# Kernel optimization log

Measured on AMD Instinct MI355X. Metric: run time of the kernel, lower is better.

Reference implementation:

```python
import jax, jax.numpy as jnp
import numpy as np

THRESHOLD = 0.5
NEG_POS_RATIO = 3


def cxcycz_to_xyz(c):
    return jnp.concatenate([c[..., :3] - c[..., 3:] / 2, c[..., :3] + c[..., 3:] / 2], axis=-1)


def xyz_to_cxcycz(x):
    return jnp.concatenate([(x[..., :3] + x[..., 3:]) / 2, x[..., 3:] - x[..., :3]], axis=-1)


def cxcycz_to_gcxgcygcz(c, priors):
    # SSD offset encoding (variance 0.1 / 0.2), 3D version
    return jnp.concatenate([
        (c[..., :3] - priors[..., :3]) / (priors[..., 3:] / 10.0),
        jnp.log(c[..., 3:] / priors[..., 3:]) * 5.0,
    ], axis=-1)


def jaccard3d(a, b):
    # a: [n,6] xyz boxes, b: [m,6] xyz boxes -> [n,m] IoU
    lo = jnp.maximum(a[:, None, :3], b[None, :, :3])
    hi = jnp.minimum(a[:, None, 3:], b[None, :, 3:])
    inter = jnp.prod(jnp.clip(hi - lo, 0.0, None), axis=-1)
    va = jnp.prod(a[:, 3:] - a[:, :3], axis=-1)
    vb = jnp.prod(b[:, 3:] - b[:, :3], axis=-1)
    return inter / (va[:, None] + vb[None, :] - inter)


def setup_inputs() -> dict:
    key = jax.random.key(0)
    ks = jax.random.split(key, 6)
    B, P, n_obj, n_classes = 16, 131072, 16, 2
    predicted_locs = jax.random.normal(ks[0], (B, P, 6), jnp.float32)
    predicted_scores = jax.random.normal(ks[1], (B, P, n_classes), jnp.float32)
    ctr = jax.random.uniform(ks[2], (B, n_obj, 3), minval=0.2, maxval=0.8)
    sz = jax.random.uniform(ks[3], (B, n_obj, 3), minval=0.05, maxval=0.2)
    boxes = jnp.concatenate([ctr - sz / 2, ctr + sz / 2], axis=-1)
    labels = jnp.ones((B, n_obj), jnp.int32)  # single foreground class (lesion)
    pctr = jax.random.uniform(ks[4], (P, 3), minval=0.0, maxval=1.0)
    psz = jax.random.uniform(ks[5], (P, 3), minval=0.05, maxval=0.3)
    priors_cxcycz = jnp.concatenate([pctr, psz], axis=-1)
    return {
        'predicted_locs': predicted_locs,
        'predicted_scores': predicted_scores,
        'boxes': boxes,
        'labels': labels,
        'priors_cxcycz': priors_cxcycz,
    }


def reference(predicted_locs, predicted_scores, boxes, labels, priors_cxcycz):
    B, P, n_classes = predicted_scores.shape
    n_obj = boxes.shape[1]
    priors_xyz = cxcycz_to_xyz(priors_cxcycz)

    def match(boxes_i, labels_i):
        ov = jaccard3d(boxes_i, priors_xyz)              # [n_obj, P]
        overlap_fp = ov.max(axis=0)                      # best overlap per prior
        object_fp = jnp.argmax(ov, axis=0)               # best object per prior
        prior_fo = jnp.argmax(ov, axis=1)                # best prior per object
        # force each object's best prior to be matched to that object
        object_fp = object_fp.at[prior_fo].set(jnp.arange(n_obj))
        overlap_fp = overlap_fp.at[prior_fo].set(1.0)
        lab = jnp.where(overlap_fp < THRESHOLD, 0, labels_i[object_fp])
        tl = cxcycz_to_gcxgcygcz(xyz_to_cxcycz(boxes_i[object_fp]), priors_cxcycz)
        return lab, tl

    true_classes, true_locs = jax.vmap(match)(boxes, labels)  # [B,P], [B,P,6]

    pos = true_classes > 0                               # [B,P]
    n_pos = pos.sum(axis=1)                              # [B]
    total_pos = n_pos.sum()

    # L1Loss(mean) over positive rows of [*,6]
    loc_abs = jnp.abs(predicted_locs - true_locs).sum(axis=-1)   # [B,P]
    loc_loss = (loc_abs * pos).sum() / (total_pos * 6).astype(predicted_locs.dtype)

    # per-prior cross-entropy
    logp = jax.nn.log_softmax(predicted_scores, axis=-1)
    conf_all = -jnp.take_along_axis(logp, true_classes[..., None], axis=-1)[..., 0]
    conf_all = jnp.where(true_classes < 0, 0.0, conf_all)  # ignored priors (soft mode only)
    conf_pos_sum = (conf_all * pos).sum()

    # hard-negative mining: zero out positives, sort each row descending, take top 3*n_pos
    conf_neg = jnp.where(pos, 0.0, conf_all)
    conf_neg_sorted = -jnp.sort(-conf_neg, axis=1)
    hard = jnp.arange(P)[None, :] < (NEG_POS_RATIO * n_pos)[:, None]
    conf_loss = (jnp.where(hard, conf_neg_sorted, 0.0).sum() + conf_pos_sum) / total_pos.astype(predicted_scores.dtype)
    return conf_loss, loc_loss
```

## Files before the change

kernel.cpp:

```cpp
#include <hip/hip_runtime.h>
#include <math.h>

#define LB 32


__device__ __forceinline__ unsigned long long umax64(unsigned long long a,
                                                     unsigned long long b) {
  return a > b ? a : b;
}

template <int NOBJ, bool FULL>
__global__ __launch_bounds__(256, 8) void mbl_match(
    const float* __restrict__ boxes, const float* __restrict__ priors,
    unsigned long long* __restrict__ prior_fo, unsigned char* __restrict__ best_u8,
    int P, int n_obj) {
  const int b = blockIdx.y;
  const int tid = threadIdx.x;
  __shared__ float4 s_box[NOBJ][2];
  __shared__ unsigned s_tr[16][264];
  for (int i = tid; i < NOBJ; i += 256) {
    float4 v0, v1;
    if (i < n_obj) {
      const float* bx = boxes + ((size_t)b * n_obj + i) * 6;
      const float l0 = bx[0], l1 = bx[1], l2 = bx[2];
      const float h0 = bx[3], h1 = bx[4], h2 = bx[5];
      v0 = make_float4(l0, l1, l2, h0);
      v1 = make_float4(h1, h2, ((h0 - l0) * (h1 - l1)) * (h2 - l2), 0.f);
    } else {
      v0 = make_float4(3e18f, 3e18f, 3e18f, 1e18f);
      v1 = make_float4(1e18f, 1e18f, 0.f, 0.f);
    }
    s_box[i][0] = v0;
    s_box[i][1] = v1;
  }
  __syncthreads();

  const int pbase = blockIdx.x * 256;
  const int p = pbase + tid;
  float lo0, lo1, lo2, hi0, hi1, hi2, vb;
  if (FULL || p < P) {
    const float2 q0 = *(const float2*)(priors + (size_t)p * 6);
    const float2 q1 = *(const float2*)(priors + (size_t)p * 6 + 2);
    const float2 q2 = *(const float2*)(priors + (size_t)p * 6 + 4);
    lo0 = q0.x - q1.y * 0.5f; hi0 = q0.x + q1.y * 0.5f;
    lo1 = q0.y - q2.x * 0.5f; hi1 = q0.y + q2.x * 0.5f;
    lo2 = q1.x - q2.y * 0.5f; hi2 = q1.x + q2.y * 0.5f;
    vb = (q1.y * q2.x) * q2.y;
  } else {
    lo0 = lo1 = lo2 = 3e18f;
    hi0 = hi1 = hi2 = 3e18f;
    vb = 0.f;
  }

  const unsigned msk = ~(unsigned)(NOBJ - 1);
  unsigned pk = 0u;

  for (int o0 = 0; o0 < NOBJ; o0 += 16) {
    if (o0) __syncthreads();
#pragma unroll
    for (int oo = 0; oo < 16; ++oo) {
      const int o = o0 + oo;
      const float4 c0 = s_box[o][0];
      const float4 c1 = s_box[o][1];
      const float d0 = fminf(c0.w, hi0) - fmaxf(c0.x, lo0);
      const float d1 = fminf(c1.x, hi1) - fmaxf(c0.y, lo1);
      const float d2 = fminf(c1.y, hi2) - fmaxf(c0.z, lo2);
      const float inter = (fmaxf(d0, 0.f) * fmaxf(d1, 0.f)) * fmaxf(d2, 0.f);
      const float un = (c1.z + vb) - inter;
      const float iou = inter * __builtin_amdgcn_rcpf(un);
      s_tr[oo][tid] = __float_as_uint(iou);
      const unsigned cand =
          (__float_as_uint(iou) & msk) | (unsigned)(NOBJ - 1 - o);
      pk = max(pk, cand);
    }
    __syncthreads();
    const int obj = tid >> 4, j = tid & 15;
    unsigned long long m = 0ULL;
#pragma unroll
    for (int i = 0; i < 16; ++i) {
      const int col = j + 16 * i;
      const unsigned long long x =
          ((unsigned long long)s_tr[obj][col] << 32) |
          (0xFFFFFFFFu - (unsigned)(pbase + col));
      m = umax64(m, x);
    }
#pragma unroll
    for (int off = 1; off < 16; off <<= 1)
      m = umax64(m, __shfl_xor(m, off, 64));
    if (j == 0) {
      const int o = o0 + obj;
      if (o < n_obj) atomicMax(&prior_fo[(size_t)b * 64 + o], m);
    }
  }

  if (FULL || p < P) {
    const int bo = (NOBJ - 1) - (int)(pk & (unsigned)(NOBJ - 1));
    best_u8[(size_t)b * P + p] =
        (unsigned char)((unsigned)bo | (pk >= 0x3F000000u ? 0x80u : 0u));
  }
}

template <int CC>
__global__ __launch_bounds__(256) void mbl_loss(
    const float* __restrict__ locs, const float* __restrict__ scores,
    const float* __restrict__ boxes, const int* __restrict__ labels,
    const float* __restrict__ priors, const unsigned long long* __restrict__ prior_fo,
    const unsigned char* __restrict__ best_u8, float* __restrict__ conf_neg,
    unsigned* __restrict__ hist0, int* __restrict__ n_pos,
    double* __restrict__ pconf, double* __restrict__ ploc, int P, int n_obj,
    int C) {
  const int b = blockIdx.y;
  const int tid = threadIdx.x;
  __shared__ float s_box[64][6];
  __shared__ int s_lab[64];
  __shared__ unsigned s_fo[64];
  __shared__ unsigned s_hist[4096];
  for (int i = tid; i < 4096; i += 256) s_hist[i] = 0u;
  for (int i = tid; i < n_obj * 6; i += 256)
    s_box[i / 6][i % 6] = boxes[(size_t)b * n_obj * 6 + i];
  for (int i = tid; i < n_obj; i += 256) {
    s_lab[i] = labels[(size_t)b * n_obj + i];
    s_fo[i] = 0xFFFFFFFFu - (unsigned)(prior_fo[(size_t)b * 64 + i] & 0xFFFFFFFFull);
  }
  __syncthreads();

  unsigned fo_r[16];
  const bool small_obj = (n_obj <= 16);
  if (small_obj) {
#pragma unroll
    for (int o = 0; o < 16; ++o) fo_r[o] = (o < n_obj) ? s_fo[o] : 0xFFFFFFFEu;
  }

  int np_l = 0;
  double cf_l = 0.0, lc_l = 0.0;

  if (CC == 2 && (P & 1) == 0) {
    const int P2 = P >> 1;
    const int chunk = (P2 + (int)gridDim.x - 1) / (int)gridDim.x;
    const int start = blockIdx.x * chunk;
    const int end = min(start + chunk, P2);
    for (int q = start + tid; q < end; q += 256) {
      const float4 sc = *(const float4*)(scores + ((size_t)b * P2 + q) * 4);
      const unsigned short bpp =
          *(const unsigned short*)(best_u8 + (size_t)b * P + 2 * q);
      float cn2[2];
#pragma unroll
      for (int e = 0; e < 2; ++e) {
        const int p = 2 * q + e;
        const unsigned bp = e ? (bpp >> 8) : (bpp & 0xFFu);
        int obj = bp & 0x7F;
        int posf = (int)(bp >> 7);
        if (small_obj) {
#pragma unroll
          for (int o = 0; o < 16; ++o)
            if (fo_r[o] == (unsigned)p) { obj = o; posf = 1; }
        } else {
          for (int o = 0; o < n_obj; ++o)
            if (s_fo[o] == (unsigned)p) { obj = o; posf = 1; }
        }
        const int lab = posf ? s_lab[obj] : 0;
        const float sx = e ? sc.z : sc.x;
        const float sy = e ? sc.w : sc.y;
        const float mm = fmaxf(sx, sy);
        const float conf =
            (lab < 0) ? 0.f
                      : (mm + __logf(__expf(sx - mm) + __expf(sy - mm)) -
                         ((lab == 0) ? sx : sy));
        float cn = conf;
        if (lab > 0) {
          np_l++;
          cf_l += (double)conf;
          const float* pr = priors + (size_t)p * 6;
          const float* pl = locs + ((size_t)b * P + p) * 6;
          float ls = 0.f;
          for (int i = 0; i < 3; ++i) {
            const float c0 = (s_box[obj][i] + s_box[obj][i + 3]) * 0.5f;
            const float szb = s_box[obj][i + 3] - s_box[obj][i];
            const float g = (c0 - pr[i]) / (pr[i + 3] / 10.0f);
            const float g2 = logf(szb / pr[i + 3]) * 5.0f;
            ls += fabsf(pl[i] - g) + fabsf(pl[i + 3] - g2);
          }
          lc_l += (double)ls;
          cn = 0.f;
        }
        cn2[e] = cn;
        atomicAdd(&s_hist[__float_as_uint(cn) >> 20], 1u);
      }
      *(float2*)(conf_neg + (size_t)b * P + 2 * q) = make_float2(cn2[0], cn2[1]);
    }
  } else {
    const int chunk = (P + (int)gridDim.x - 1) / (int)gridDim.x;
    const int start = blockIdx.x * chunk;
    const int end = min(start + chunk, P);
    for (int p = start + tid; p < end; p += 256) {
      const unsigned char bp = best_u8[(size_t)b * P + p];
      int obj = bp & 0x7F;
      int posf = bp >> 7;
      for (int o = 0; o < n_obj; ++o)
        if (s_fo[o] == (unsigned)p) { obj = o; posf = 1; }
      const int lab = posf ? s_lab[obj] : 0;
      const float* sp = scores + ((size_t)b * P + p) * C;
      float m = sp[0];
      for (int c = 1; c < C; ++c) m = fmaxf(m, sp[c]);
      float se = 0.f;
      for (int c = 0; c < C; ++c) se += __expf(sp[c] - m);
      const float conf = (lab < 0) ? 0.f : (m + __logf(se) - sp[lab]);
      float cn = conf;
      if (lab > 0) {
        np_l++;
        cf_l += (double)conf;
        const float* pr = priors + (size_t)p * 6;
        const float* pl = locs + ((size_t)b * P + p) * 6;
        float ls = 0.f;
        for (int i = 0; i < 3; ++i) {
          const float c0 = (s_box[obj][i] + s_box[obj][i + 3]) * 0.5f;
          const float szb = s_box[obj][i + 3] - s_box[obj][i];
          const float g = (c0 - pr[i]) / (pr[i + 3] / 10.0f);
          const float g2 = logf(szb / pr[i + 3]) * 5.0f;
          ls += fabsf(pl[i] - g) + fabsf(pl[i + 3] - g2);
        }
        lc_l += (double)ls;
        cn = 0.f;
      }
      conf_neg[(size_t)b * P + p] = cn;
      atomicAdd(&s_hist[__float_as_uint(cn) >> 20], 1u);
    }
  }

  __shared__ int r_np[256];
  __shared__ double r_c[256];
  __shared__ double r_l[256];
  r_np[tid] = np_l;
  r_c[tid] = cf_l;
  r_l[tid] = lc_l;
  __syncthreads();
  for (int s = 128; s > 0; s >>= 1) {
    if (tid < s) {
      r_np[tid] += r_np[tid + s];
      r_c[tid] += r_c[tid + s];
      r_l[tid] += r_l[tid + s];
    }
    __syncthreads();
  }
  if (tid == 0 && r_np[0] > 0) {
    atomicAdd(&n_pos[b], r_np[0]);
    atomicAdd(&pconf[b], r_c[0]);
    atomicAdd(&ploc[b], r_l[0]);
  }
  for (int i = tid; i < 4096; i += 256)
    if (s_hist[i]) atomicAdd(&hist0[(size_t)b * 4096 + i], s_hist[i]);
}

template <int BINS>
__device__ void block_select(const unsigned* __restrict__ h, int remk,
                             unsigned* s_scan, int* s_out, unsigned* sel,
                             int* remk_o) {
  constexpr int BPT = BINS / 256;
  const int t = threadIdx.x;
  if (t == 0) { s_out[0] = BINS - 1; s_out[1] = 0; }
  unsigned mb[BPT];
  unsigned s = 0;
#pragma unroll
  for (int i = 0; i < BPT; ++i) { mb[i] = h[t * BPT + i]; s += mb[i]; }
  unsigned incl = s;
  s_scan[t] = incl;
  __syncthreads();
  for (int off = 1; off < 256; off <<= 1) {
    const unsigned add = (t >= off) ? s_scan[t - off] : 0u;
    __syncthreads();
    incl += add;
    s_scan[t] = incl;
    __syncthreads();
  }
  const unsigned total = s_scan[255];
  const unsigned R = total - incl;
  if (remk > 0 && R < (unsigned)remk && R + s >= (unsigned)remk) {
    unsigned acc = R;
    int sel_i = t * BPT, rk = 0;
    bool done = false;
#pragma unroll
    for (int i = BPT - 1; i >= 0; --i) {
      if (!done && acc + mb[i] >= (unsigned)remk) {
        sel_i = t * BPT + i;
// ... 117 lines not shown
  const float* locs = (const float*)d_in[0];
  const float* scores = (const float*)d_in[1];
  const float* boxes = (const float*)d_in[2];
  const int* labels = (const int*)d_in[3];
  const float* priors = (const float*)d_in[4];

  const long long sz_locs = (long long)in_sizes[0];
  const long long sz_scores = (long long)in_sizes[1];
  const long long sz_priors = (long long)in_sizes[4];
  const int P = (int)(sz_priors / 6);
  const int B = (int)(sz_locs / sz_priors);
  const int n_obj = in_sizes[3] / B;
  const int C = (int)(sz_scores * 6 / sz_locs);

  char* ws = (char*)d_ws;
  size_t off = 0;
  double* pconf = (double*)(ws + off); off += (size_t)B * 8;
  double* ploc = (double*)(ws + off); off += (size_t)B * 8;
  double* phard = (double*)(ws + off); off += (size_t)B * 8;
  int* n_pos = (int*)(ws + off); off += ((size_t)B * 4 + 15) & ~(size_t)15;
  unsigned* counter = (unsigned*)(ws + off); off += 16;
  unsigned long long* prior_fo = (unsigned long long*)(ws + off);
  off += (size_t)B * 64 * 8;
  unsigned* hist0 = (unsigned*)(ws + off); off += (size_t)B * 4096 * 4;
  unsigned* hist1 = (unsigned*)(ws + off); off += (size_t)B * 4096 * 4;
  const size_t zero_bytes = off;
  float* conf_neg = (float*)(ws + off); off += ((size_t)B * P * 4 + 15) & ~(size_t)15;
  unsigned char* best_u8 = (unsigned char*)(ws + off);
  off += ((size_t)B * P + 15) & ~(size_t)15;
  (void)ws_size;

  hipMemsetAsync(d_ws, 0, zero_bytes, stream);

  const int nblk = (P + 255) / 256;
  const dim3 mgrid(nblk, B);
  const bool full = (P % 256) == 0;
  if (n_obj <= 16) {
    if (full) mbl_match<16, true><<<mgrid, 256, 0, stream>>>(boxes, priors, prior_fo, best_u8, P, n_obj);
    else      mbl_match<16, false><<<mgrid, 256, 0, stream>>>(boxes, priors, prior_fo, best_u8, P, n_obj);
  } else if (n_obj <= 32) {
    if (full) mbl_match<32, true><<<mgrid, 256, 0, stream>>>(boxes, priors, prior_fo, best_u8, P, n_obj);
    else      mbl_match<32, false><<<mgrid, 256, 0, stream>>>(boxes, priors, prior_fo, best_u8, P, n_obj);
  } else {
    if (full) mbl_match<64, true><<<mgrid, 256, 0, stream>>>(boxes, priors, prior_fo, best_u8, P, n_obj);
    else      mbl_match<64, false><<<mgrid, 256, 0, stream>>>(boxes, priors, prior_fo, best_u8, P, n_obj);
  }

  const dim3 lgrid(LB, B);
  if (C == 2)
    mbl_loss<2><<<lgrid, 256, 0, stream>>>(locs, scores, boxes, labels, priors,
                                           prior_fo, best_u8, conf_neg, hist0, n_pos,
                                           pconf, ploc, P, n_obj, C);
  else
    mbl_loss<0><<<lgrid, 256, 0, stream>>>(locs, scores, boxes, labels, priors,
                                           prior_fo, best_u8, conf_neg, hist0, n_pos,
                                           pconf, ploc, P, n_obj, C);

  mbl_hist1<<<lgrid, 256, 0, stream>>>(conf_neg, n_pos, hist0, hist1, P);
  mbl_sum<<<lgrid, 256, 0, stream>>>(conf_neg, n_pos, hist0, hist1, pconf, ploc,
                                     phard, counter, P, B, (float*)d_out);
}
```

Measured before the change: 102.9 us.

## Process two priors per thread in match kernel with scalar box loads

The match kernel now handles two priors per thread (a 512-prior tile) and loads the ground-truth boxes through readfirstlane scalar reads instead of a shared-memory box table. Objects are processed in passes of 8. Each thread first reduces its two priors' IoUs and records which one won in a bitmask, so the shared-memory transpose and the per-object block reduction are half the size. The aim is fewer blocks, less shared-memory traffic and fewer atomics per prior, at the cost of more registers, with the 8-occupancy launch bound dropped. The old mbl_match is left behind as a stub that no longer writes best_u8, and the launch sites call mbl_match2 instead.

```diff
diff --git a/kernel.cpp b/kernel.cpp
--- a/kernel.cpp
+++ b/kernel.cpp
@@ -1,6 +1,8 @@
 #include <hip/hip_runtime.h>
 #include <math.h>
 
+#define MITEMS 2
+#define TILE 512
 #define LB 32
 
 
@@ -8,95 +10,234 @@
                                                      unsigned long long b) {
   return a > b ? a : b;
 }
+__device__ __forceinline__ float rfl(float x) {
+  return __uint_as_float(__builtin_amdgcn_readfirstlane(__float_as_uint(x)));
+}
 
 template <int NOBJ, bool FULL>
-__global__ __launch_bounds__(256, 8) void mbl_match(
+__global__ __launch_bounds__(256) void mbl_match(
     const float* __restrict__ boxes, const float* __restrict__ priors,
     unsigned long long* __restrict__ prior_fo, unsigned char* __restrict__ best_u8,
     int P, int n_obj) {
   const int b = blockIdx.y;
   const int tid = threadIdx.x;
-  __shared__ float4 s_box[NOBJ][2];
-  __shared__ unsigned s_tr[16][264];
-  for (int i = tid; i < NOBJ; i += 256) {
-    float4 v0, v1;
-    if (i < n_obj) {
-      const float* bx = boxes + ((size_t)b * n_obj + i) * 6;
-      const float l0 = bx[0], l1 = bx[1], l2 = bx[2];
-      const float h0 = bx[3], h1 = bx[4], h2 = bx[5];
-      v0 = make_float4(l0, l1, l2, h0);
-      v1 = make_float4(h1, h2, ((h0 - l0) * (h1 - l1)) * (h2 - l2), 0.f);
+  __shared__ unsigned s_iou[8][264];
+  __shared__ unsigned s_kfl[264];
+
+  const int pbase = blockIdx.x * TILE;
+  float lo0[MITEMS], lo1[MITEMS], lo2[MITEMS], hi0[MITEMS], hi1[MITEMS],
+      hi2[MITEMS], vb[MITEMS];
+#pragma unroll
+  for (int k = 0; k < MITEMS; ++k) {
+    const int p = pbase + k * 256 + tid;
+    if (FULL || p < P) {
+      const float2 q0 = *(const float2*)(priors + (size_t)p * 6);
+      const float2 q1 = *(const float2*)(priors + (size_t)p * 6 + 2);
+      const float2 q2 = *(const float2*)(priors + (size_t)p * 6 + 4);
+      lo0[k] = q0.x - q1.y * 0.5f; hi0[k] = q0.x + q1.y * 0.5f;
+      lo1[k] = q0.y - q2.x * 0.5f; hi1[k] = q0.y + q2.x * 0.5f;
+      lo2[k] = q1.x - q2.y * 0.5f; hi2[k] = q1.x + q2.y * 0.5f;
+      vb[k] = (q1.y * q2.x) * q2.y;
     } else {
-      v0 = make_float4(3e18f, 3e18f, 3e18f, 1e18f);
-      v1 = make_float4(1e18f, 1e18f, 0.f, 0.f);
-    }
-    s_box[i][0] = v0;
-    s_box[i][1] = v1;
-  }
-  __syncthreads();
-
-  const int pbase = blockIdx.x * 256;
-  const int p = pbase + tid;
-  float lo0, lo1, lo2, hi0, hi1, hi2, vb;
-  if (FULL || p < P) {
-    const float2 q0 = *(const float2*)(priors + (size_t)p * 6);
-    const float2 q1 = *(const float2*)(priors + (size_t)p * 6 + 2);
-    const float2 q2 = *(const float2*)(priors + (size_t)p * 6 + 4);
-    lo0 = q0.x - q1.y * 0.5f; hi0 = q0.x + q1.y * 0.5f;
-    lo1 = q0.y - q2.x * 0.5f; hi1 = q0.y + q2.x * 0.5f;
-    lo2 = q1.x - q2.y * 0.5f; hi2 = q1.x + q2.y * 0.5f;
-    vb = (q1.y * q2.x) * q2.y;
-  } else {
-    lo0 = lo1 = lo2 = 3e18f;
-    hi0 = hi1 = hi2 = 3e18f;
-    vb = 0.f;
+      lo0[k] = lo1[k] = lo2[k] = 3e18f;
+      hi0[k] = hi1[k] = hi2[k] = 3e18f;
+      vb[k] = 0.f;
+    }
   }
 
   const unsigned msk = ~(unsigned)(NOBJ - 1);
   unsigned pk = 0u;
-
-  for (int o0 = 0; o0 < NOBJ; o0 += 16) {
-    if (o0) __syncthreads();
-#pragma unroll
-    for (int oo = 0; oo < 16; ++oo) {
-      const int o = o0 + oo;
-      const float4 c0 = s_box[o][0];
-      const float4 c1 = s_box[o][1];
-      const float d0 = fminf(c0.w, hi0) - fmaxf(c0.x, lo0);
-      const float d1 = fminf(c1.x, hi1) - fmaxf(c0.y, lo1);
-      const float d2 = fminf(c1.y, hi2) - fmaxf(c0.z, lo2);
-      const float inter = (fmaxf(d0, 0.f) * fmaxf(d1, 0.f)) * fmaxf(d2, 0.f);
-      const float un = (c1.z + vb) - inter;
-      const float iou = inter * __builtin_amdgcn_rcpf(un);
-      s_tr[oo][tid] = __float_as_uint(iou);
-      const unsigned cand =
-          (__float_as_uint(iou) & msk) | (unsigned)(NOBJ - 1 - o);
-      pk = max(pk, cand);
-    }
+  const float* bx = boxes + (size_t)b * n_obj * 6;
+
+  for (int pass = 0; pass < NOBJ / 8; ++pass) {
+    if (pass) __syncthreads();
+    float sl0[8], sl1[8], sl2[8], sh0[8], sh1[8], sh2[8], sv[8];
+#pragma unroll
+    for (int oo = 0; oo < 8; ++oo) {
+      const int o = pass * 8 + oo;
+      if (o < n_obj) {
+        const float* q = bx + (size_t)o * 6;
+        sl0[oo] = rfl(q[0]); sl1[oo] = rfl(q[1]); sl2[oo] = rfl(q[2]);
+        sh0[oo] = rfl(q[3]); sh1[oo] = rfl(q[4]); sh2[oo] = rfl(q[5]);
+        sv[oo] = rfl(((sh0[oo] - sl0[oo]) * (sh1[oo] - sl1[oo])) *
+                     (sh2[oo] - sl2[oo]));
+      } else {
+        sl0[oo] = sl1[oo] = sl2[oo] = 3e18f;
+        sh0[oo] = sh1[oo] = sh2[oo] = 3e18f;
+        sv[oo] = 0.f;
+      }
+    }
+
+    float piou[8];
+#pragma unroll
+    for (int oo = 0; oo < 8; ++oo) piou[oo] = 0.f;
+    unsigned kfl = 0u;
+
+#pragma unroll
+    for (int oo = 0; oo < 8; ++oo) {
+      const int o = pass * 8 + oo;
+#pragma unroll
+      for (int k = 0; k < MITEMS; ++k) {
+        const float d0 = fminf(sh0[oo], hi0[k]) - fmaxf(sl0[oo], lo0[k]);
+        const float d1 = fminf(sh1[oo], hi1[k]) - fmaxf(sl1[oo], lo1[k]);
+        const float d2 = fminf(sh2[oo], hi2[k]) - fmaxf(sl2[oo], lo2[k]);
+        const float inter = (fmaxf(d0, 0.f) * fmaxf(d1, 0.f)) * fmaxf(d2, 0.f);
+        const float un = (sv[oo] + vb[k]) - inter;
+        const float iou = inter * __builtin_amdgcn_rcpf(un);
+        const unsigned cand =
+            (__float_as_uint(iou) & msk) | (unsigned)(NOBJ - 1 - o);
+        pk = max(pk, cand);
+        const bool win = iou > piou[oo];
+        piou[oo] = win ? iou : piou[oo];
+        if (k > 0) kfl = win ? (kfl | (1u << oo)) : kfl;
+      }
+    }
+
+    s_kfl[tid] = kfl;
+#pragma unroll
+    for (int oo = 0; oo < 8; ++oo) s_iou[oo][tid] = __float_as_uint(piou[oo]);
     __syncthreads();
-    const int obj = tid >> 4, j = tid & 15;
+    const int obj8 = tid >> 5, j = tid & 31;
     unsigned long long m = 0ULL;
 #pragma unroll
-    for (int i = 0; i < 16; ++i) {
-      const int col = j + 16 * i;
-      const unsigned long long x =
-          ((unsigned long long)s_tr[obj][col] << 32) |
-          (0xFFFFFFFFu - (unsigned)(pbase + col));
-      m = umax64(m, x);
-    }
-#pragma unroll
-    for (int off = 1; off < 16; off <<= 1)
+    for (int i = 0; i < 8; ++i) {
+      const int col = j + 32 * i;
+      const unsigned ib = s_iou[obj8][col];
+      const unsigned kf = (s_kfl[col] >> obj8) & 1u;
+      const int p = pbase + (int)kf * 256 + col;
+      m = umax64(m, ((unsigned long long)ib << 32) |
+                        (0xFFFFFFFFu - (unsigned)p));
+    }
+#pragma unroll
+    for (int off = 1; off < 32; off <<= 1)
       m = umax64(m, __shfl_xor(m, off, 64));
     if (j == 0) {
-      const int o = o0 + obj;
+      const int o = pass * 8 + obj8;
       if (o < n_obj) atomicMax(&prior_fo[(size_t)b * 64 + o], m);
     }
   }
 
-  if (FULL || p < P) {
-    const int bo = (NOBJ - 1) - (int)(pk & (unsigned)(NOBJ - 1));
-    best_u8[(size_t)b * P + p] =
-        (unsigned char)((unsigned)bo | (pk >= 0x3F000000u ? 0x80u : 0u));
+#pragma unroll
+  for (int k = 0; k < MITEMS; ++k) {
+    const int p = pbase + k * 256 + tid;
+    if (FULL || p < P) {
+    }
+  }
+  (void)best_u8;
+}
+
+template <int NOBJ, bool FULL>
+__global__ __launch_bounds__(256) void mbl_match2(
+    const float* __restrict__ boxes, const float* __restrict__ priors,
+    unsigned long long* __restrict__ prior_fo, unsigned char* __restrict__ best_u8,
+    int P, int n_obj) {
+  const int b = blockIdx.y;
+  const int tid = threadIdx.x;
+  __shared__ unsigned s_iou[8][264];
+  __shared__ unsigned s_kfl[264];
+
+  const int pbase = blockIdx.x * TILE;
+  float lo0[MITEMS], lo1[MITEMS], lo2[MITEMS], hi0[MITEMS], hi1[MITEMS],
+      hi2[MITEMS], vb[MITEMS];
+#pragma unroll
+  for (int k = 0; k < MITEMS; ++k) {
+    const int p = pbase + k * 256 + tid;
+    if (FULL || p < P) {
+      const float2 q0 = *(const float2*)(priors + (size_t)p * 6);
+      const float2 q1 = *(const float2*)(priors + (size_t)p * 6 + 2);
+      const float2 q2 = *(const float2*)(priors + (size_t)p * 6 + 4);
+      lo0[k] = q0.x - q1.y * 0.5f; hi0[k] = q0.x + q1.y * 0.5f;
+      lo1[k] = q0.y - q2.x * 0.5f; hi1[k] = q0.y + q2.x * 0.5f;
+      lo2[k] = q1.x - q2.y * 0.5f; hi2[k] = q1.x + q2.y * 0.5f;
+      vb[k] = (q1.y * q2.x) * q2.y;
+    } else {
+      lo0[k] = lo1[k] = lo2[k] = 3e18f;
+      hi0[k] = hi1[k] = hi2[k] = 3e18f;
+      vb[k] = 0.f;
+    }
+  }
+
+  const unsigned msk = ~(unsigned)(NOBJ - 1);
+  unsigned pk[MITEMS];
+#pragma unroll
+  for (int k = 0; k < MITEMS; ++k) pk[k] = 0u;
+  const float* bx = boxes + (size_t)b * n_obj * 6;
+
+  for (int pass = 0; pass < NOBJ / 8; ++pass) {
+    if (pass) __syncthreads();
+    float sl0[8], sl1[8], sl2[8], sh0[8], sh1[8], sh2[8], sv[8];
+#pragma unroll
+    for (int oo = 0; oo < 8; ++oo) {
+      const int o = pass * 8 + oo;
+      if (o < n_obj) {
+        const float* q = bx + (size_t)o * 6;
+        sl0[oo] = rfl(q[0]); sl1[oo] = rfl(q[1]); sl2[oo] = rfl(q[2]);
+        sh0[oo] = rfl(q[3]); sh1[oo] = rfl(q[4]); sh2[oo] = rfl(q[5]);
+        sv[oo] = rfl(((sh0[oo] - sl0[oo]) * (sh1[oo] - sl1[oo])) *
+                     (sh2[oo] - sl2[oo]));
+      } else {
+        sl0[oo] = sl1[oo] = sl2[oo] = 3e18f;
+        sh0[oo] = sh1[oo] = sh2[oo] = 3e18f;
+        sv[oo] = 0.f;
+      }
+    }
+
+    float piou[8];
+#pragma unroll
+    for (int oo = 0; oo < 8; ++oo) piou[oo] = 0.f;
+    unsigned kfl = 0u;
+
+#pragma unroll
+    for (int oo = 0; oo < 8; ++oo) {
+      const int o = pass * 8 + oo;
+      const unsigned inv_o = (unsigned)(NOBJ - 1 - o);
+#pragma unroll
+      for (int k = 0; k < MITEMS; ++k) {
+        const float d0 = fminf(sh0[oo], hi0[k]) - fmaxf(sl0[oo], lo0[k]);
+        const float d1 = fminf(sh1[oo], hi1[k]) - fmaxf(sl1[oo], lo1[k]);
+        const float d2 = fminf(sh2[oo], hi2[k]) - fmaxf(sl2[oo], lo2[k]);
+        const float inter = (fmaxf(d0, 0.f) * fmaxf(d1, 0.f)) * fmaxf(d2, 0.f);
+        const float un = (sv[oo] + vb[k]) - inter;
+        const float iou = inter * __builtin_amdgcn_rcpf(un);
+        pk[k] = max(pk[k], (__float_as_uint(iou) & msk) | inv_o);
+        const bool win = iou > piou[oo];
+        piou[oo] = win ? iou : piou[oo];
+        if (k > 0) kfl = win ? (kfl | (1u << oo)) : kfl;
+      }
+    }
+
+    s_kfl[tid] = kfl;
+#pragma unroll
+    for (int oo = 0; oo < 8; ++oo) s_iou[oo][tid] = __float_as_uint(piou[oo]);
+    __syncthreads();
+    const int obj8 = tid >> 5, j = tid & 31;
+    unsigned long long m = 0ULL;
+#pragma unroll
+    for (int i = 0; i < 8; ++i) {
+      const int col = j + 32 * i;
+      const unsigned ib = s_iou[obj8][col];
+      const unsigned kf = (s_kfl[col] >> obj8) & 1u;
+      const int p = pbase + (int)kf * 256 + col;
+      m = umax64(m, ((unsigned long long)ib << 32) |
+                        (0xFFFFFFFFu - (unsigned)p));
+    }
+#pragma unroll
+    for (int off = 1; off < 32; off <<= 1)
+      m = umax64(m, __shfl_xor(m, off, 64));
+    if (j == 0) {
+      const int o = pass * 8 + obj8;
+      if (o < n_obj) atomicMax(&prior_fo[(size_t)b * 64 + o], m);
+    }
+  }
+
+#pragma unroll
+  for (int k = 0; k < MITEMS; ++k) {
+    const int p = pbase + k * 256 + tid;
+    if (FULL || p < P) {
+      const int bo = (NOBJ - 1) - (int)(pk[k] & (unsigned)(NOBJ - 1));
+      best_u8[(size_t)b * P + p] =
+          (unsigned char)((unsigned)bo | (pk[k] >= 0x3F000000u ? 0x80u : 0u));
+    }
   }
 }
 
@@ -432,18 +573,18 @@
 
   hipMemsetAsync(d_ws, 0, zero_bytes, stream);
 
-  const int nblk = (P + 255) / 256;
+  const int nblk = (P + TILE - 1) / TILE;
   const dim3 mgrid(nblk, B);
-  const bool full = (P % 256) == 0;
+  const bool full = (P % TILE) == 0;
   if (n_obj <= 16) {
-    if (full) mbl_match<16, true><<<mgrid, 256, 0, stream>>>(boxes, priors, prior_fo, best_u8, P, n_obj);
-    else      mbl_match<16, false><<<mgrid, 256, 0, stream>>>(boxes, priors, prior_fo, best_u8, P, n_obj);
+    if (full) mbl_match2<16, true><<<mgrid, 256, 0, stream>>>(boxes, priors, prior_fo, best_u8, P, n_obj);
+    else      mbl_match2<16, false><<<mgrid, 256, 0, stream>>>(boxes, priors, prior_fo, best_u8, P, n_obj);
   } else if (n_obj <= 32) {
-    if (full) mbl_match<32, true><<<mgrid, 256, 0, stream>>>(boxes, priors, prior_fo, best_u8, P, n_obj);
-    else      mbl_match<32, false><<<mgrid, 256, 0, stream>>>(boxes, priors, prior_fo, best_u8, P, n_obj);
+    if (full) mbl_match2<32, true><<<mgrid, 256, 0, stream>>>(boxes, priors, prior_fo, best_u8, P, n_obj);
+    else      mbl_match2<32, false><<<mgrid, 256, 0, stream>>>(boxes, priors, prior_fo, best_u8, P, n_obj);
   } else {
-    if (full) mbl_match<64, true><<<mgrid, 256, 0, stream>>>(boxes, priors, prior_fo, best_u8, P, n_obj);
-    else      mbl_match<64, false><<<mgrid, 256, 0, stream>>>(boxes, priors, prior_fo, best_u8, P, n_obj);
+    if (full) mbl_match2<64, true><<<mgrid, 256, 0, stream>>>(boxes, priors, prior_fo, best_u8, P, n_obj);
+    else      mbl_match2<64, false><<<mgrid, 256, 0, stream>>>(boxes, priors, prior_fo, best_u8, P, n_obj);
   }
 
   const dim3 lgrid(LB, B);
```

Result: faster. 97.96 us (-4.8%).

## Fuse prior matching with loss kernel and patch forced matches in a fixup pass

Applied to the files above, without the earlier changes.

The separate match and loss kernels are merged into one kernel. It computes IoU per prior against boxes held in scalar registers, then applies cross-entropy, localisation loss and the histogram update in the same pass. The per-object best prior is gathered with a per-thread running max and a single block reduction per group of eight objects, instead of a shared-memory transpose at every tile. Because the forced prior-to-object assignment is only known after all blocks finish, a small single-thread fixup kernel per batch then adjusts conf_neg, hist0, n_pos and the partial sums for those priors. This removes one kernel launch and the best_u8/conf_neg round trip, but the fixup runs serially and the grid is smaller (64×B blocks), which may reduce parallelism.

```diff
diff --git a/kernel.cpp b/kernel.cpp
--- a/kernel.cpp
+++ b/kernel.cpp
@@ -1,6 +1,7 @@
 #include <hip/hip_runtime.h>
 #include <math.h>
 
+#define LBF 64
 #define LB 32
 
 
@@ -8,174 +9,126 @@
                                                      unsigned long long b) {
   return a > b ? a : b;
 }
-
-template <int NOBJ, bool FULL>
-__global__ __launch_bounds__(256, 8) void mbl_match(
-    const float* __restrict__ boxes, const float* __restrict__ priors,
-    unsigned long long* __restrict__ prior_fo, unsigned char* __restrict__ best_u8,
-    int P, int n_obj) {
+__device__ __forceinline__ float rfl(float x) {
+  return __uint_as_float(__builtin_amdgcn_readfirstlane(__float_as_uint(x)));
+}
+
+template <int CC>
+__global__ __launch_bounds__(256) void mbl_fused(
+    const float* __restrict__ locs, const float* __restrict__ scores,
+    const float* __restrict__ boxes, const int* __restrict__ labels,
+    const float* __restrict__ priors, unsigned long long* __restrict__ prior_fo,
+    unsigned char* __restrict__ best_u8, float* __restrict__ conf_neg,
+    unsigned* __restrict__ hist0, int* __restrict__ n_pos,
+    double* __restrict__ pconf, double* __restrict__ ploc, int P, int n_obj,
+    int chunks, int C) {
   const int b = blockIdx.y;
   const int tid = threadIdx.x;
-  __shared__ float4 s_box[NOBJ][2];
-  __shared__ unsigned s_tr[16][264];
-  for (int i = tid; i < NOBJ; i += 256) {
-    float4 v0, v1;
-    if (i < n_obj) {
-      const float* bx = boxes + ((size_t)b * n_obj + i) * 6;
-      const float l0 = bx[0], l1 = bx[1], l2 = bx[2];
-      const float h0 = bx[3], h1 = bx[4], h2 = bx[5];
-      v0 = make_float4(l0, l1, l2, h0);
-      v1 = make_float4(h1, h2, ((h0 - l0) * (h1 - l1)) * (h2 - l2), 0.f);
-    } else {
-      v0 = make_float4(3e18f, 3e18f, 3e18f, 1e18f);
-      v1 = make_float4(1e18f, 1e18f, 0.f, 0.f);
-    }
-    s_box[i][0] = v0;
-    s_box[i][1] = v1;
-  }
-  __syncthreads();
-
-  const int pbase = blockIdx.x * 256;
-  const int p = pbase + tid;
-  float lo0, lo1, lo2, hi0, hi1, hi2, vb;
-  if (FULL || p < P) {
-    const float2 q0 = *(const float2*)(priors + (size_t)p * 6);
-    const float2 q1 = *(const float2*)(priors + (size_t)p * 6 + 2);
-    const float2 q2 = *(const float2*)(priors + (size_t)p * 6 + 4);
-    lo0 = q0.x - q1.y * 0.5f; hi0 = q0.x + q1.y * 0.5f;
-    lo1 = q0.y - q2.x * 0.5f; hi1 = q0.y + q2.x * 0.5f;
-    lo2 = q1.x - q2.y * 0.5f; hi2 = q1.x + q2.y * 0.5f;
-    vb = (q1.y * q2.x) * q2.y;
-  } else {
-    lo0 = lo1 = lo2 = 3e18f;
-    hi0 = hi1 = hi2 = 3e18f;
-    vb = 0.f;
-  }
-
-  const unsigned msk = ~(unsigned)(NOBJ - 1);
-  unsigned pk = 0u;
-
-  for (int o0 = 0; o0 < NOBJ; o0 += 16) {
-    if (o0) __syncthreads();
-#pragma unroll
-    for (int oo = 0; oo < 16; ++oo) {
-      const int o = o0 + oo;
-      const float4 c0 = s_box[o][0];
-      const float4 c1 = s_box[o][1];
-      const float d0 = fminf(c0.w, hi0) - fmaxf(c0.x, lo0);
-      const float d1 = fminf(c1.x, hi1) - fmaxf(c0.y, lo1);
-      const float d2 = fminf(c1.y, hi2) - fmaxf(c0.z, lo2);
-      const float inter = (fmaxf(d0, 0.f) * fmaxf(d1, 0.f)) * fmaxf(d2, 0.f);
-      const float un = (c1.z + vb) - inter;
-      const float iou = inter * __builtin_amdgcn_rcpf(un);
-      s_tr[oo][tid] = __float_as_uint(iou);
-      const unsigned cand =
-          (__float_as_uint(iou) & msk) | (unsigned)(NOBJ - 1 - o);
-      pk = max(pk, cand);
-    }
-    __syncthreads();
-    const int obj = tid >> 4, j = tid & 15;
-    unsigned long long m = 0ULL;
-#pragma unroll
-    for (int i = 0; i < 16; ++i) {
-      const int col = j + 16 * i;
-      const unsigned long long x =
-          ((unsigned long long)s_tr[obj][col] << 32) |
-          (0xFFFFFFFFu - (unsigned)(pbase + col));
-      m = umax64(m, x);
-    }
-#pragma unroll
-    for (int off = 1; off < 16; off <<= 1)
-      m = umax64(m, __shfl_xor(m, off, 64));
-    if (j == 0) {
-      const int o = o0 + obj;
-      if (o < n_obj) atomicMax(&prior_fo[(size_t)b * 64 + o], m);
-    }
-  }
-
-  if (FULL || p < P) {
-    const int bo = (NOBJ - 1) - (int)(pk & (unsigned)(NOBJ - 1));
-    best_u8[(size_t)b * P + p] =
-        (unsigned char)((unsigned)bo | (pk >= 0x3F000000u ? 0x80u : 0u));
-  }
-}
-
-template <int CC>
-__global__ __launch_bounds__(256) void mbl_loss(
-    const float* __restrict__ locs, const float* __restrict__ scores,
-    const float* __restrict__ boxes, const int* __restrict__ labels,
-    const float* __restrict__ priors, const unsigned long long* __restrict__ prior_fo,
-    const unsigned char* __restrict__ best_u8, float* __restrict__ conf_neg,
-    unsigned* __restrict__ hist0, int* __restrict__ n_pos,
-    double* __restrict__ pconf, double* __restrict__ ploc, int P, int n_obj,
-    int C) {
-  const int b = blockIdx.y;
-  const int tid = threadIdx.x;
-  __shared__ float s_box[64][6];
+  __shared__ unsigned s_hist[4096];
+  __shared__ unsigned s_iou[8][264];
+  __shared__ unsigned s_pinv[8][264];
   __shared__ int s_lab[64];
-  __shared__ unsigned s_fo[64];
-  __shared__ unsigned s_hist[4096];
   for (int i = tid; i < 4096; i += 256) s_hist[i] = 0u;
-  for (int i = tid; i < n_obj * 6; i += 256)
-    s_box[i / 6][i % 6] = boxes[(size_t)b * n_obj * 6 + i];
-  for (int i = tid; i < n_obj; i += 256) {
-    s_lab[i] = labels[(size_t)b * n_obj + i];
-    s_fo[i] = 0xFFFFFFFFu - (unsigned)(prior_fo[(size_t)b * 64 + i] & 0xFFFFFFFFull);
-  }
-  __syncthreads();
-
-  unsigned fo_r[16];
-  const bool small_obj = (n_obj <= 16);
-  if (small_obj) {
-#pragma unroll
-    for (int o = 0; o < 16; ++o) fo_r[o] = (o < n_obj) ? s_fo[o] : 0xFFFFFFFEu;
-  }
+  if (tid < 64) s_lab[tid] = (tid < n_obj) ? labels[(size_t)b * n_obj + tid] : 0;
+  __syncthreads();
+
+  const int base = blockIdx.x * chunks * 256;
+  const float* bx = boxes + (size_t)b * n_obj * 6;
+  const size_t rowb = (size_t)b * P;
+  const unsigned msk = ~63u;
 
   int np_l = 0;
   double cf_l = 0.0, lc_l = 0.0;
-
-  if (CC == 2 && (P & 1) == 0) {
-    const int P2 = P >> 1;
-    const int chunk = (P2 + (int)gridDim.x - 1) / (int)gridDim.x;
-    const int start = blockIdx.x * chunk;
-    const int end = min(start + chunk, P2);
-    for (int q = start + tid; q < end; q += 256) {
-      const float4 sc = *(const float4*)(scores + ((size_t)b * P2 + q) * 4);
-      const unsigned short bpp =
-          *(const unsigned short*)(best_u8 + (size_t)b * P + 2 * q);
-      float cn2[2];
-#pragma unroll
-      for (int e = 0; e < 2; ++e) {
-        const int p = 2 * q + e;
-        const unsigned bp = e ? (bpp >> 8) : (bpp & 0xFFu);
-        int obj = bp & 0x7F;
-        int posf = (int)(bp >> 7);
-        if (small_obj) {
-#pragma unroll
-          for (int o = 0; o < 16; ++o)
-            if (fo_r[o] == (unsigned)p) { obj = o; posf = 1; }
+  const int COHS = (n_obj + 7) / 8;
+
+  for (int coh = 0; coh < COHS; ++coh) {
+    float sl0[8], sl1[8], sl2[8], sh0[8], sh1[8], sh2[8], sv[8];
+#pragma unroll
+    for (int oo = 0; oo < 8; ++oo) {
+      const int o = coh * 8 + oo;
+      if (o < n_obj) {
+        const float* q = bx + (size_t)o * 6;
+        sl0[oo] = rfl(q[0]); sl1[oo] = rfl(q[1]); sl2[oo] = rfl(q[2]);
+        sh0[oo] = rfl(q[3]); sh1[oo] = rfl(q[4]); sh2[oo] = rfl(q[5]);
+        sv[oo] = rfl(((sh0[oo] - sl0[oo]) * (sh1[oo] - sl1[oo])) *
+                     (sh2[oo] - sl2[oo]));
+      } else {
+        sl0[oo] = sl1[oo] = sl2[oo] = 3e18f;
+        sh0[oo] = sh1[oo] = sh2[oo] = 3e18f;
+        sv[oo] = 0.f;
+      }
+    }
+    float piou[8];
+    unsigned pinv[8];
+#pragma unroll
+    for (int oo = 0; oo < 8; ++oo) { piou[oo] = 0.f; pinv[oo] = 0u; }
+
+    const bool lastc = (coh == COHS - 1);
+    for (int c = 0; c < chunks; ++c) {
+      const int p = base + c * 256 + tid;
+      const bool act = p < P;
+      float lo0, lo1, lo2, hi0, hi1, hi2, vb;
+      if (act) {
+        const float2 q0 = *(const float2*)(priors + (size_t)p * 6);
+        const float2 q1 = *(const float2*)(priors + (size_t)p * 6 + 2);
+        const float2 q2 = *(const float2*)(priors + (size_t)p * 6 + 4);
+        lo0 = q0.x - q1.y * 0.5f; hi0 = q0.x + q1.y * 0.5f;
+        lo1 = q0.y - q2.x * 0.5f; hi1 = q0.y + q2.x * 0.5f;
+        lo2 = q1.x - q2.y * 0.5f; hi2 = q1.x + q2.y * 0.5f;
+        vb = (q1.y * q2.x) * q2.y;
+      } else {
+        lo0 = lo1 = lo2 = hi0 = hi1 = hi2 = 3e18f;
+        vb = 0.f;
+      }
+      unsigned pk = 0u;
+      if (coh > 0 && act) pk = __float_as_uint(conf_neg[rowb + p]);
+      const unsigned invp = 0xFFFFFFFFu - (unsigned)p;
+#pragma unroll
+      for (int oo = 0; oo < 8; ++oo) {
+        const int o = coh * 8 + oo;
+        const float d0 = fminf(sh0[oo], hi0) - fmaxf(sl0[oo], lo0);
+        const float d1 = fminf(sh1[oo], hi1) - fmaxf(sl1[oo], lo1);
+        const float d2 = fminf(sh2[oo], hi2) - fmaxf(sl2[oo], lo2);
+        const float inter = (fmaxf(d0, 0.f) * fmaxf(d1, 0.f)) * fmaxf(d2, 0.f);
+        const float un = (sv[oo] + vb) - inter;
+        const float iou = inter * __builtin_amdgcn_rcpf(un);
+        pk = max(pk, (__float_as_uint(iou) & msk) | (unsigned)(63 - o));
+        const bool win = iou > piou[oo];
+        piou[oo] = win ? iou : piou[oo];
+        pinv[oo] = win ? invp : pinv[oo];
+      }
+      if (!lastc) {
+        if (act) conf_neg[rowb + p] = __uint_as_float(pk);
+      } else if (act) {
+        const int bo = 63 - (int)(pk & 63u);
+        const int posf = pk >= 0x3F000000u;
+        const int lab = posf ? s_lab[bo] : 0;
+        float conf;
+        if (CC == 2) {
+          const float2 sc = *(const float2*)(scores + (rowb + p) * 2);
+          const float mm = fmaxf(sc.x, sc.y);
+          conf = (lab < 0) ? 0.f
+                           : (mm + __logf(__expf(sc.x - mm) + __expf(sc.y - mm)) -
+                              ((lab == 0) ? sc.x : sc.y));
         } else {
-          for (int o = 0; o < n_obj; ++o)
-            if (s_fo[o] == (unsigned)p) { obj = o; posf = 1; }
+          const float* sp = scores + (rowb + p) * C;
+          float m = sp[0];
+          for (int cc = 1; cc < C; ++cc) m = fmaxf(m, sp[cc]);
+          float se = 0.f;
+          for (int cc = 0; cc < C; ++cc) se += __expf(sp[cc] - m);
+          conf = (lab < 0) ? 0.f : (m + __logf(se) - sp[lab]);
         }
-        const int lab = posf ? s_lab[obj] : 0;
-        const float sx = e ? sc.z : sc.x;
-        const float sy = e ? sc.w : sc.y;
-        const float mm = fmaxf(sx, sy);
-        const float conf =
-            (lab < 0) ? 0.f
-                      : (mm + __logf(__expf(sx - mm) + __expf(sy - mm)) -
-                         ((lab == 0) ? sx : sy));
         float cn = conf;
         if (lab > 0) {
           np_l++;
           cf_l += (double)conf;
           const float* pr = priors + (size_t)p * 6;
-          const float* pl = locs + ((size_t)b * P + p) * 6;
+          const float* pl = locs + (rowb + p) * 6;
           float ls = 0.f;
           for (int i = 0; i < 3; ++i) {
-            const float c0 = (s_box[obj][i] + s_box[obj][i + 3]) * 0.5f;
-            const float szb = s_box[obj][i + 3] - s_box[obj][i];
+            const float bl = bx[bo * 6 + i], bh = bx[bo * 6 + i + 3];
+            const float c0 = (bl + bh) * 0.5f;
+            const float szb = bh - bl;
             const float g = (c0 - pr[i]) / (pr[i + 3] / 10.0f);
             const float g2 = logf(szb / pr[i + 3]) * 5.0f;
             ls += fabsf(pl[i] - g) + fabsf(pl[i + 3] - g2);
@@ -183,47 +136,34 @@
           lc_l += (double)ls;
           cn = 0.f;
         }
-        cn2[e] = cn;
+        conf_neg[rowb + p] = cn;
         atomicAdd(&s_hist[__float_as_uint(cn) >> 20], 1u);
-      }
-      *(float2*)(conf_neg + (size_t)b * P + 2 * q) = make_float2(cn2[0], cn2[1]);
-    }
-  } else {
-    const int chunk = (P + (int)gridDim.x - 1) / (int)gridDim.x;
-    const int start = blockIdx.x * chunk;
-    const int end = min(start + chunk, P);
-    for (int p = start + tid; p < end; p += 256) {
-      const unsigned char bp = best_u8[(size_t)b * P + p];
-      int obj = bp & 0x7F;
-      int posf = bp >> 7;
-      for (int o = 0; o < n_obj; ++o)
-        if (s_fo[o] == (unsigned)p) { obj = o; posf = 1; }
-      const int lab = posf ? s_lab[obj] : 0;
-      const float* sp = scores + ((size_t)b * P + p) * C;
-      float m = sp[0];
-      for (int c = 1; c < C; ++c) m = fmaxf(m, sp[c]);
-      float se = 0.f;
-      for (int c = 0; c < C; ++c) se += __expf(sp[c] - m);
-      const float conf = (lab < 0) ? 0.f : (m + __logf(se) - sp[lab]);
-      float cn = conf;
-      if (lab > 0) {
-        np_l++;
-        cf_l += (double)conf;
-        const float* pr = priors + (size_t)p * 6;
-        const float* pl = locs + ((size_t)b * P + p) * 6;
-        float ls = 0.f;
-        for (int i = 0; i < 3; ++i) {
-          const float c0 = (s_box[obj][i] + s_box[obj][i + 3]) * 0.5f;
-          const float szb = s_box[obj][i + 3] - s_box[obj][i];
-          const float g = (c0 - pr[i]) / (pr[i + 3] / 10.0f);
-          const float g2 = logf(szb / pr[i + 3]) * 5.0f;
-          ls += fabsf(pl[i] - g) + fabsf(pl[i + 3] - g2);
-        }
-        lc_l += (double)ls;
-        cn = 0.f;
-      }
-      conf_neg[(size_t)b * P + p] = cn;
-      atomicAdd(&s_hist[__float_as_uint(cn) >> 20], 1u);
+        best_u8[rowb + p] =
+            (unsigned char)((unsigned)bo | (posf ? 0x80u : 0u));
+      }
+    }
+
+    __syncthreads();
+#pragma unroll
+    for (int oo = 0; oo < 8; ++oo) {
+      s_iou[oo][tid] = __float_as_uint(piou[oo]);
+      s_pinv[oo][tid] = pinv[oo];
+    }
+    __syncthreads();
+    const int obj8 = tid >> 5, j = tid & 31;
+    unsigned long long m = 0ULL;
+#pragma unroll
+    for (int i = 0; i < 8; ++i) {
+      const int col = j + 32 * i;
+      m = umax64(m, ((unsigned long long)s_iou[obj8][col] << 32) |
+                        s_pinv[obj8][col]);
+    }
+#pragma unroll
+    for (int off = 1; off < 32; off <<= 1)
+      m = umax64(m, __shfl_xor(m, off, 64));
+    if (j == 0) {
+      const int o = coh * 8 + obj8;
+      if (o < n_obj) atomicMax(&prior_fo[(size_t)b * 64 + o], m);
     }
   }
 
@@ -249,6 +189,77 @@
   }
   for (int i = tid; i < 4096; i += 256)
     if (s_hist[i]) atomicAdd(&hist0[(size_t)b * 4096 + i], s_hist[i]);
+}
+
+__global__ void mbl_fixup(
+    const float* __restrict__ locs, const float* __restrict__ scores,
+    const float* __restrict__ boxes, const int* __restrict__ labels,
+    const float* __restrict__ priors,
+    const unsigned long long* __restrict__ prior_fo,
+    const unsigned char* __restrict__ best_u8, float* __restrict__ conf_neg,
+    unsigned* __restrict__ hist0, int* __restrict__ n_pos,
+    double* __restrict__ pconf, double* __restrict__ ploc, int P, int n_obj,
+    int C) {
+  const int b = blockIdx.x;
+  if (threadIdx.x != 0) return;
+  const size_t rowb = (size_t)b * P;
+  unsigned fp[64];
+  for (int o = 0; o < n_obj; ++o)
+    fp[o] = 0xFFFFFFFFu - (unsigned)(prior_fo[(size_t)b * 64 + o] & 0xFFFFFFFFull);
+  int d_np = 0;
+  double d_cf = 0.0, d_lc = 0.0;
+  for (int o = 0; o < n_obj; ++o) {
+    const unsigned p = fp[o];
+    if (p >= (unsigned)P) continue;
+    bool last = true;
+    for (int o2 = o + 1; o2 < n_obj; ++o2)
+      if (fp[o2] == p) { last = false; break; }
+    if (!last) continue;
+    const unsigned char bp = best_u8[rowb + p];
+    const int obj_o = bp & 0x7F;
+    const int posf_o = bp >> 7;
+    if (posf_o && obj_o == o) continue;
+    const int lab_old = posf_o ? labels[(size_t)b * n_obj + obj_o] : 0;
+    const int lab_new = labels[(size_t)b * n_obj + o];
+    const float* sp = scores + (rowb + p) * C;
+    float m = sp[0];
+    for (int cc = 1; cc < C; ++cc) m = fmaxf(m, sp[cc]);
+    float se = 0.f;
+    for (int cc = 0; cc < C; ++cc) se += __expf(sp[cc] - m);
+    const float lse = m + __logf(se);
+    const float cn_old = conf_neg[rowb + p];
+    float cn_new = 0.f;
+    if (lab_new == 0) cn_new = lse - sp[0];
+    if (__float_as_uint(cn_new) != __float_as_uint(cn_old)) {
+      hist0[(size_t)b * 4096 + (__float_as_uint(cn_old) >> 20)] -= 1u;
+      hist0[(size_t)b * 4096 + (__float_as_uint(cn_new) >> 20)] += 1u;
+      conf_neg[rowb + p] = cn_new;
+    }
+    d_np += (lab_new > 0) - (lab_old > 0);
+    const float* pr = priors + (size_t)p * 6;
+    const float* pl = locs + (rowb + p) * 6;
+    for (int which = 0; which < 2; ++which) {
+      const int lab = which ? lab_new : lab_old;
+      const int obj = which ? o : obj_o;
+      if (lab <= 0) continue;
+      const double sgn = which ? 1.0 : -1.0;
+      d_cf += sgn * (double)(lse - sp[lab]);
+      const float* q = boxes + ((size_t)b * n_obj + obj) * 6;
+      float ls = 0.f;
+      for (int i = 0; i < 3; ++i) {
+        const float bl = q[i], bh = q[i + 3];
+        const float c0 = (bl + bh) * 0.5f;
+        const float szb = bh - bl;
+        const float g = (c0 - pr[i]) / (pr[i + 3] / 10.0f);
+        const float g2 = logf(szb / pr[i + 3]) * 5.0f;
+        ls += fabsf(pl[i] - g) + fabsf(pl[i + 3] - g2);
+      }
+      d_lc += sgn * (double)ls;
+    }
+  }
+  if (d_np) n_pos[b] += d_np;
+  pconf[b] += d_cf;
+  ploc[b] += d_lc;
 }
 
 template <int BINS>
@@ -432,30 +443,23 @@
 
   hipMemsetAsync(d_ws, 0, zero_bytes, stream);
 
-  const int nblk = (P + 255) / 256;
-  const dim3 mgrid(nblk, B);
-  const bool full = (P % 256) == 0;
-  if (n_obj <= 16) {
-    if (full) mbl_match<16, true><<<mgrid, 256, 0, stream>>>(boxes, priors, prior_fo, best_u8, P, n_obj);
-    else      mbl_match<16, false><<<mgrid, 256, 0, stream>>>(boxes, priors, prior_fo, best_u8, P, n_obj);
-  } else if (n_obj <= 32) {
-    if (full) mbl_match<32, true><<<mgrid, 256, 0, stream>>>(boxes, priors, prior_fo, best_u8, P, n_obj);
-    else      mbl_match<32, false><<<mgrid, 256, 0, stream>>>(boxes, priors, prior_fo, best_u8, P, n_obj);
-  } else {
-    if (full) mbl_match<64, true><<<mgrid, 256, 0, stream>>>(boxes, priors, prior_fo, best_u8, P, n_obj);
-    else      mbl_match<64, false><<<mgrid, 256, 0, stream>>>(boxes, priors, prior_fo, best_u8, P, n_obj);
-  }
+  const int tileF = LBF * 256;
+  const int chunks = (P + tileF - 1) / tileF;
+  const dim3 fgrid(LBF, B);
+  if (C == 2)
+    mbl_fused<2><<<fgrid, 256, 0, stream>>>(locs, scores, boxes, labels, priors,
+                                            prior_fo, best_u8, conf_neg, hist0,
+                                            n_pos, pconf, ploc, P, n_obj, chunks, C);
+  else
+    mbl_fused<0><<<fgrid, 256, 0, stream>>>(locs, scores, boxes, labels, priors,
+                                            prior_fo, best_u8, conf_neg, hist0,
+                                            n_pos, pconf, ploc, P, n_obj, chunks, C);
+
+  mbl_fixup<<<B, 64, 0, stream>>>(locs, scores, boxes, labels, priors, prior_fo,
+                                  best_u8, conf_neg, hist0, n_pos, pconf, ploc,
+                                  P, n_obj, C);
 
   const dim3 lgrid(LB, B);
-  if (C == 2)
-    mbl_loss<2><<<lgrid, 256, 0, stream>>>(locs, scores, boxes, labels, priors,
-                                           prior_fo, best_u8, conf_neg, hist0, n_pos,
-                                           pconf, ploc, P, n_obj, C);
-  else
-    mbl_loss<0><<<lgrid, 256, 0, stream>>>(locs, scores, boxes, labels, priors,
-                                           prior_fo, best_u8, conf_neg, hist0, n_pos,
-                                           pconf, ploc, P, n_obj, C);
-
   mbl_hist1<<<lgrid, 256, 0, stream>>>(conf_neg, n_pos, hist0, hist1, P);
   mbl_sum<<<lgrid, 256, 0, stream>>>(conf_neg, n_pos, hist0, hist1, pconf, ploc,
                                      phard, counter, P, B, (float*)d_out);
```

New measurement: 128.9 us. 25.2% more time.

## Process two priors per thread in match kernel with in-register per-object reduction

Applied to the files above, without the earlier changes.

Each thread in the match kernel now handles two priors, so each block covers 512 priors and each shared box load is reused twice. Per-object best (IoU, prior) pairs are first reduced in registers across the thread's priors, then written in groups of 8 objects to shared memory for block reduction. This halves the number of blocks and global atomics and does less LDS traffic per prior. In exchange it adds more register pressure, drops the occupancy hint, and uses more passes with barriers. The per-prior best object is now tracked with a float compare instead of packed-integer max, which may break ties differently.

```diff
diff --git a/kernel.cpp b/kernel.cpp
--- a/kernel.cpp
+++ b/kernel.cpp
@@ -1,6 +1,8 @@
 #include <hip/hip_runtime.h>
 #include <math.h>
 
+#define MITEMS 2
+#define TILE 512
 #define LB 32
 
 
@@ -10,14 +12,15 @@
 }
 
 template <int NOBJ, bool FULL>
-__global__ __launch_bounds__(256, 8) void mbl_match(
+__global__ __launch_bounds__(256) void mbl_match(
     const float* __restrict__ boxes, const float* __restrict__ priors,
     unsigned long long* __restrict__ prior_fo, unsigned char* __restrict__ best_u8,
     int P, int n_obj) {
   const int b = blockIdx.y;
   const int tid = threadIdx.x;
   __shared__ float4 s_box[NOBJ][2];
-  __shared__ unsigned s_tr[16][264];
+  __shared__ unsigned s_iou[8][264];
+  __shared__ unsigned s_pinv[8][264];
   for (int i = tid; i < NOBJ; i += 256) {
     float4 v0, v1;
     if (i < n_obj) {
@@ -35,68 +38,91 @@
   }
   __syncthreads();
 
-  const int pbase = blockIdx.x * 256;
-  const int p = pbase + tid;
-  float lo0, lo1, lo2, hi0, hi1, hi2, vb;
-  if (FULL || p < P) {
-    const float2 q0 = *(const float2*)(priors + (size_t)p * 6);
-    const float2 q1 = *(const float2*)(priors + (size_t)p * 6 + 2);
-    const float2 q2 = *(const float2*)(priors + (size_t)p * 6 + 4);
-    lo0 = q0.x - q1.y * 0.5f; hi0 = q0.x + q1.y * 0.5f;
-    lo1 = q0.y - q2.x * 0.5f; hi1 = q0.y + q2.x * 0.5f;
-    lo2 = q1.x - q2.y * 0.5f; hi2 = q1.x + q2.y * 0.5f;
-    vb = (q1.y * q2.x) * q2.y;
-  } else {
-    lo0 = lo1 = lo2 = 3e18f;
-    hi0 = hi1 = hi2 = 3e18f;
-    vb = 0.f;
-  }
-
-  const unsigned msk = ~(unsigned)(NOBJ - 1);
-  unsigned pk = 0u;
-
-  for (int o0 = 0; o0 < NOBJ; o0 += 16) {
-    if (o0) __syncthreads();
-#pragma unroll
-    for (int oo = 0; oo < 16; ++oo) {
-      const int o = o0 + oo;
+  const int pbase = blockIdx.x * TILE;
+  float lo0[MITEMS], lo1[MITEMS], lo2[MITEMS], hi0[MITEMS], hi1[MITEMS],
+      hi2[MITEMS], vb[MITEMS];
+  unsigned invp[MITEMS];
+#pragma unroll
+  for (int k = 0; k < MITEMS; ++k) {
+    const int p = pbase + k * 256 + tid;
+    if (FULL || p < P) {
+      const float2 q0 = *(const float2*)(priors + (size_t)p * 6);
+      const float2 q1 = *(const float2*)(priors + (size_t)p * 6 + 2);
+      const float2 q2 = *(const float2*)(priors + (size_t)p * 6 + 4);
+      lo0[k] = q0.x - q1.y * 0.5f; hi0[k] = q0.x + q1.y * 0.5f;
+      lo1[k] = q0.y - q2.x * 0.5f; hi1[k] = q0.y + q2.x * 0.5f;
+      lo2[k] = q1.x - q2.y * 0.5f; hi2[k] = q1.x + q2.y * 0.5f;
+      vb[k] = (q1.y * q2.x) * q2.y;
+      invp[k] = 0xFFFFFFFFu - (unsigned)p;
+    } else {
+      lo0[k] = lo1[k] = lo2[k] = 3e18f;
+      hi0[k] = hi1[k] = hi2[k] = 3e18f;
+      vb[k] = 0.f;
+      invp[k] = 0u;
+    }
+  }
+
+  float bv[MITEMS];
+  int bo[MITEMS];
+#pragma unroll
+  for (int k = 0; k < MITEMS; ++k) { bv[k] = -1.0f; bo[k] = 0; }
+
+  for (int pass = 0; pass < NOBJ / 8; ++pass) {
+    if (pass) __syncthreads();
+    float piou[8];
+    unsigned pinv[8];
+#pragma unroll
+    for (int oo = 0; oo < 8; ++oo) { piou[oo] = 0.f; pinv[oo] = 0u; }
+
+#pragma unroll
+    for (int oo = 0; oo < 8; ++oo) {
+      const int o = pass * 8 + oo;
       const float4 c0 = s_box[o][0];
       const float4 c1 = s_box[o][1];
-      const float d0 = fminf(c0.w, hi0) - fmaxf(c0.x, lo0);
-      const float d1 = fminf(c1.x, hi1) - fmaxf(c0.y, lo1);
-      const float d2 = fminf(c1.y, hi2) - fmaxf(c0.z, lo2);
-      const float inter = (fmaxf(d0, 0.f) * fmaxf(d1, 0.f)) * fmaxf(d2, 0.f);
-      const float un = (c1.z + vb) - inter;
-      const float iou = inter * __builtin_amdgcn_rcpf(un);
-      s_tr[oo][tid] = __float_as_uint(iou);
-      const unsigned cand =
-          (__float_as_uint(iou) & msk) | (unsigned)(NOBJ - 1 - o);
-      pk = max(pk, cand);
+#pragma unroll
+      for (int k = 0; k < MITEMS; ++k) {
+        const float d0 = fminf(c0.w, hi0[k]) - fmaxf(c0.x, lo0[k]);
+        const float d1 = fminf(c1.x, hi1[k]) - fmaxf(c0.y, lo1[k]);
+        const float d2 = fminf(c1.y, hi2[k]) - fmaxf(c0.z, lo2[k]);
+        const float inter = (fmaxf(d0, 0.f) * fmaxf(d1, 0.f)) * fmaxf(d2, 0.f);
+        const float un = (c1.z + vb[k]) - inter;
+        const float iou = inter * __builtin_amdgcn_rcpf(un);
+        if (iou > bv[k]) { bv[k] = iou; bo[k] = o; }
+        const bool win = iou > piou[oo];
+        piou[oo] = win ? iou : piou[oo];
+        pinv[oo] = win ? invp[k] : pinv[oo];
+      }
+    }
+
+#pragma unroll
+    for (int oo = 0; oo < 8; ++oo) {
+      s_iou[oo][tid] = __float_as_uint(piou[oo]);
+      s_pinv[oo][tid] = pinv[oo];
     }
     __syncthreads();
-    const int obj = tid >> 4, j = tid & 15;
+    const int obj8 = tid >> 5, j = tid & 31;
     unsigned long long m = 0ULL;
 #pragma unroll
-    for (int i = 0; i < 16; ++i) {
-      const int col = j + 16 * i;
-      const unsigned long long x =
-          ((unsigned long long)s_tr[obj][col] << 32) |
-          (0xFFFFFFFFu - (unsigned)(pbase + col));
-      m = umax64(m, x);
-    }
-#pragma unroll
-    for (int off = 1; off < 16; off <<= 1)
+    for (int i = 0; i < 8; ++i) {
+      const int col = j + 32 * i;
+      m = umax64(m, ((unsigned long long)s_iou[obj8][col] << 32) |
+                        s_pinv[obj8][col]);
+    }
+#pragma unroll
+    for (int off = 1; off < 32; off <<= 1)
       m = umax64(m, __shfl_xor(m, off, 64));
     if (j == 0) {
-      const int o = o0 + obj;
+      const int o = pass * 8 + obj8;
       if (o < n_obj) atomicMax(&prior_fo[(size_t)b * 64 + o], m);
     }
   }
 
-  if (FULL || p < P) {
-    const int bo = (NOBJ - 1) - (int)(pk & (unsigned)(NOBJ - 1));
-    best_u8[(size_t)b * P + p] =
-        (unsigned char)((unsigned)bo | (pk >= 0x3F000000u ? 0x80u : 0u));
+#pragma unroll
+  for (int k = 0; k < MITEMS; ++k) {
+    const int p = pbase + k * 256 + tid;
+    if (FULL || p < P)
+      best_u8[(size_t)b * P + p] =
+          (unsigned char)((unsigned)bo[k] | (bv[k] >= 0.5f ? 0x80u : 0u));
   }
 }
 
@@ -432,9 +458,9 @@
 
   hipMemsetAsync(d_ws, 0, zero_bytes, stream);
 
-  const int nblk = (P + 255) / 256;
+  const int nblk = (P + TILE - 1) / TILE;
   const dim3 mgrid(nblk, B);
-  const bool full = (P % 256) == 0;
+  const bool full = (P % TILE) == 0;
   if (n_obj <= 16) {
     if (full) mbl_match<16, true><<<mgrid, 256, 0, stream>>>(boxes, priors, prior_fo, best_u8, P, n_obj);
     else      mbl_match<16, false><<<mgrid, 256, 0, stream>>>(boxes, priors, prior_fo, best_u8, P, n_obj);
```

New measurement: 92.41 us. -10.2%, faster.
